# Optimization experiments

Hardware: AMD Instinct MI355X
Metric: run time of the kernel (lower is better)

Reference implementation:

```python
import jax, jax.numpy as jnp
import numpy as np

B, S, D = 8, 2048, 1024          # batch, seq, d_model
E, H = 32, 128                   # n_experts_ffn, d_expert_ffn
SHARED, K = 2, 4                 # n_expert_shared_ffn, k_ffn (routed top-k)
R = E - SHARED                   # n_expert_routed_ffn


def setup_inputs() -> dict:
    key = jax.random.key(0)
    ks = jax.random.split(key, 5)
    token_stream = jax.random.normal(ks[0], (B, S, D), jnp.float32)
    selection_input = jax.random.normal(ks[1], (B, S, D), jnp.float32)
    # init scaling mirrors reset_parameters (std_scale = 1)
    keys = jax.random.normal(ks[2], (E, D, H), jnp.float32) / np.sqrt(D)
    values = jax.random.normal(ks[3], (E, H, D), jnp.float32) / np.sqrt(E * H)
    expert_sel = jax.random.normal(ks[4], (E, D), jnp.float32) / np.sqrt(D)
    bias_ffn = jnp.zeros((E,), jnp.float32)
    return {
        "token_stream": token_stream,
        "selection_input": selection_input,
        "keys": keys,
        "values": values,
        "expert_sel": expert_sel,
        "bias_ffn": bias_ffn,
    }


def reference(token_stream, selection_input, keys, values, expert_sel, bias_ffn):
    # Router: sigmoid affinity over all experts. [B,S,E]
    affinity = jax.nn.sigmoid(jnp.einsum("bsd,ed->bse", selection_input, expert_sel))

    # Top-k over routed experts only (bias-corrected scores pick INDICES only).
    routed_scores = affinity[..., :R] + bias_ffn[:R]
    _, sel_routed = jax.lax.top_k(routed_scores, K)            # [B,S,K] int32
    shared = jnp.broadcast_to(jnp.arange(R, E, dtype=sel_routed.dtype),
                              sel_routed.shape[:-1] + (SHARED,))
    sel = jnp.concatenate([sel_routed, shared], axis=-1)        # [B,S,K+SHARED]

    # Gather the (unbiased) affinities of the selected experts.
    aff_sel = jnp.take_along_axis(affinity, sel, axis=-1)       # [B,S,K+SHARED]

    # Per-token dense combine weight over experts: w[b,s,e] = affinity if e selected else 0.
    # (selected indices are distinct: topk indices in [0,R), shared in [R,E))
    w = jnp.sum(jax.nn.one_hot(sel, E, dtype=affinity.dtype) * aff_sel[..., None],
                axis=-2)                                        # [B,S,E]

    # Expert FFN: cvmm(x, sel, keys) -> silu -> cvmm(., sel, values) weighted by affinity.
    # Dense-masked equivalent: compute all experts, zero out unselected via w.
    h = jax.nn.silu(jnp.einsum("bsd,edh->bseh", token_stream, keys))  # [B,S,E,H]
    out = jnp.einsum("bseh,bse,ehd->bsd", h, w, values)               # [B,S,D]
    return out, sel
```

## Files before the change

### kernel.cpp

```cpp
#include <hip/hip_runtime.h>
#include <math.h>

#define NTOK   16384
#define DDIM   1024
#define HDIM   128
#define NEXP   32
#define NROUTE 30
#define TOPK   4
#define TS     64
#define NJOBS_F 1696
#define CPX_F   212
#define SLAB   ((size_t)NTOK * DDIM)

typedef short bf16x8 __attribute__((ext_vector_type(8)));
typedef float f32x16 __attribute__((ext_vector_type(16)));
typedef unsigned int u32x4 __attribute__((ext_vector_type(4)));
typedef unsigned short u16;

__device__ __forceinline__ float sigmoidf_(float x) { return 1.f / (1.f + expf(-x)); }

__device__ __forceinline__ u16 f2bf(float x) {
  unsigned u = __float_as_uint(x);
  u += 0x7fffu + ((u >> 16) & 1u);
  return (u16)(u >> 16);
}
__device__ __forceinline__ float bf2f(u16 v) {
  return __uint_as_float(((unsigned)v) << 16);
}

__device__ __forceinline__ f32x16 mfma32(uint4 a, uint4 b, f32x16 c) {
  union { uint4 u; bf16x8 h; } A, B;
  A.u = a; B.u = b;
  return __builtin_amdgcn_mfma_f32_32x32x16_bf16(A.h, B.h, c, 0, 0, 0);
}

__device__ __forceinline__ void gload16(const void* g, void* l) {
  __builtin_amdgcn_global_load_lds(
      (const __attribute__((address_space(1))) unsigned int*)g,
      (__attribute__((address_space(3))) unsigned int*)l, 16, 0, 0);
}

__device__ __forceinline__ void lgkm_bar() {
  asm volatile("s_waitcnt lgkmcnt(0)\ns_barrier" ::: "memory");
}

__global__ __launch_bounds__(256) void prep_all_kernel(
    const float* __restrict__ X, u16* __restrict__ Xb,
    const float* __restrict__ K, u16* __restrict__ Kf,
    const float* __restrict__ V, u16* __restrict__ Vf)
{
  __shared__ float t[128][129];
  const int tid = threadIdx.x;
  int b = blockIdx.x;

  if (b < 4096) {
    const size_t base = ((size_t)b * 256 + tid) * 16;
    u16 v[16];
#pragma unroll
    for (int i = 0; i < 4; ++i) {
      const float4 f = *(const float4*)(X + base + i * 4);
      v[i*4+0] = f2bf(f.x); v[i*4+1] = f2bf(f.y);
      v[i*4+2] = f2bf(f.z); v[i*4+3] = f2bf(f.w);
    }
    *(uint4*)(Xb + base) = *(const uint4*)v;
    *(uint4*)(Xb + base + 8) = *(const uint4*)(v + 8);
    return;
  }
  b -= 4096;
  if (b < 256) {
    const int kc = b & 7, e = b >> 3;
#pragma unroll
    for (int i = 0; i < 64; ++i) {
      const int g = tid + i * 256;
      const int d = g >> 7, h = g & 127;
      t[d][h] = K[((size_t)e * DDIM + kc * 128 + d) * HDIM + h];
    }
    __syncthreads();
    u16* dst = Kf + ((size_t)e * 8 + kc) * 16384;
#pragma unroll
    for (int i = 0; i < 64; ++i) {
      const int f = tid + i * 256;
      const int s = f >> 11, wn = (f >> 9) & 3, l = (f >> 3) & 63, j = f & 7;
      const int khalf = l >> 5, l31 = l & 31;
      dst[f] = f2bf(t[(s * 2 + khalf) * 8 + j][wn * 32 + l31]);
    }
    return;
  }
  b -= 256;
  {
    const int dc = b & 7, e = b >> 3;
#pragma unroll
    for (int i = 0; i < 64; ++i) {
      const int g = tid + i * 256;
      const int h = g >> 7, dl = g & 127;
      t[h][dl] = V[((size_t)e * HDIM + h) * DDIM + dc * 128 + dl];
    }
    __syncthreads();
    u16* dst = Vf + ((size_t)e * 8 + dc) * 16384;
#pragma unroll
    for (int i = 0; i < 64; ++i) {
      const int f = tid + i * 256;
      const int s = f >> 11, wn = (f >> 9) & 3, l = (f >> 3) & 63, j = f & 7;
      const int khalf = l >> 5, l31 = l & 31;
      dst[f] = f2bf(t[(s * 2 + khalf) * 8 + j][wn * 32 + l31]);
    }
  }
}

__global__ __launch_bounds__(256, 4) void router_kernel(
    const float* __restrict__ SI, const float* __restrict__ ES,
    const float* __restrict__ bias, float* __restrict__ out_sel,
    float* __restrict__ w6, int* __restrict__ sel_e, int* __restrict__ counts)
{
  __shared__ float pbuf[4][32][65];
  __shared__ float aff[16][33];
  const int tid = threadIdx.x, wave = tid >> 6, lane = tid & 63;
  const int tok0 = blockIdx.x * 16 + wave * 4;

  float x[4][16];
#pragma unroll
  for (int t = 0; t < 4; ++t) {
    const float* xp = SI + (size_t)(tok0 + t) * DDIM + lane * 16;
#pragma unroll
    for (int q = 0; q < 4; ++q) {
      const float4 v = *(const float4*)(xp + q * 4);
      x[t][q*4+0]=v.x; x[t][q*4+1]=v.y; x[t][q*4+2]=v.z; x[t][q*4+3]=v.w;
    }
  }

#pragma unroll
  for (int g = 0; g < 4; ++g) {
#pragma unroll
    for (int ei = 0; ei < 8; ++ei) {
      const int e = g * 8 + ei;
      float es[16];
      const float* ep = ES + (size_t)e * DDIM + lane * 16;
#pragma unroll
      for (int q = 0; q < 4; ++q) {
        const float4 v = *(const float4*)(ep + q * 4);
        es[q*4+0]=v.x; es[q*4+1]=v.y; es[q*4+2]=v.z; es[q*4+3]=v.w;
      }
#pragma unroll
      for (int t = 0; t < 4; ++t) {
        float p = 0.f;
#pragma unroll
        for (int u = 0; u < 16; ++u) p = fmaf(x[t][u], es[u], p);
        pbuf[wave][ei * 4 + t][lane] = p;
      }
    }
    const int pr = lane & 31, hf = lane >> 5;
    const float* src = &pbuf[wave][pr][hf * 32];
    float4 s4 = make_float4(0.f, 0.f, 0.f, 0.f);
#pragma unroll
    for (int j = 0; j < 8; ++j) {
      const float4 v = *(const float4*)(src + j * 4);
      s4.x += v.x; s4.y += v.y; s4.z += v.z; s4.w += v.w;
    }
    float s = (s4.x + s4.y) + (s4.z + s4.w);
    s += __shfl_xor(s, 32, 64);
    if (hf == 0) aff[wave * 4 + (pr & 3)][g * 8 + (pr >> 2)] = s;
  }

  if (lane < 4) {
    const int tok = tok0 + lane;
    float af[NEXP];
#pragma unroll
    for (int e2 = 0; e2 < NEXP; ++e2)
      af[e2] = sigmoidf_(aff[wave * 4 + lane][e2]);
    float sc[NROUTE];
#pragma unroll
    for (int e2 = 0; e2 < NROUTE; ++e2) sc[e2] = af[e2] + bias[e2];
    unsigned used = 0u;
    int idx[6];
#pragma unroll
    for (int j = 0; j < TOPK; ++j) {
      float bv = -1e30f; int best = 0;
#pragma unroll
      for (int e2 = 0; e2 < NROUTE; ++e2)
        if (!((used >> e2) & 1u) && sc[e2] > bv) { bv = sc[e2]; best = e2; }
      used |= (1u << best);
      idx[j] = best;
    }
    idx[4] = 30; idx[5] = 31;
#pragma unroll
    for (int j = 0; j < 6; ++j) {
      out_sel[(size_t)tok * 6 + j] = (float)idx[j];
      w6[(size_t)tok * 6 + j] = af[idx[j]];
    }
#pragma unroll
    for (int j = 0; j < TOPK; ++j) {
      sel_e[(size_t)tok * TOPK + j] = idx[j];
      atomicAdd(&counts[j * NEXP + idx[j]], 1);
    }
  }
}

__global__ __launch_bounds__(256) void scan_kernel(const int* __restrict__ counts,
                                                   int* __restrict__ offsets,
                                                   int4* __restrict__ jm)
{
  __shared__ int c4[30][4];
  __shared__ int off4[30][4];
  __shared__ int nch[32];
  __shared__ int joff[31];
  const int tid = threadIdx.x;

  if (tid < 4) {
    int off = 0;
    for (int e = 0; e < NROUTE; ++e) {
      const int c = counts[tid * NEXP + e];
      offsets[tid * NEXP + e] = off;
      c4[e][tid] = c; off4[e][tid] = off;
      off += c;
    }
  }
  __syncthreads();
  if (tid < NROUTE) {
    int n = 0;
#pragma unroll
    for (int r = 0; r < 4; ++r) n += (c4[tid][r] + TS - 1) / TS;
    nch[tid] = n;
  }
  __syncthreads();
  if (tid == 0) {
    int run = 0;
    for (int e = 0; e < NROUTE; ++e) { joff[e] = run; run += nch[e]; }
    joff[NROUTE] = run;
  }
  __syncthreads();
  const int rt = joff[NROUTE];

  if (tid < NROUTE) {
    const int e = tid;
    int idx = joff[e];
    for (int r = 0; r < 4; ++r) {
      const int c = c4[e][r];
      for (int ch = 0; ch * TS < c; ++ch)
        jm[idx++] = make_int4(e, off4[e][r] + ch * TS, min(TS, c - ch * TS), r);
    }
  }
  for (int i = tid; i < 512; i += 256)
    jm[rt + i] = make_int4(30 + (i >> 8), (i & 255) * TS, TS, 4 + (i >> 8));
  for (int i = rt + 512 + tid; i < NJOBS_F; i += 256)
    jm[i] = make_int4(0, 0, 0, 0);
}

__global__ __launch_bounds__(256) void scatter_kernel(
    const int* __restrict__ sel_e, const float* __restrict__ w6,
    const int* __restrict__ offsets, int* __restrict__ cursor,
    int* __restrict__ list_tok, float* __restrict__ list_w)
{
  const int t = blockIdx.x * 256 + threadIdx.x;
  if (t >= NTOK) return;
#pragma unroll
  for (int j = 0; j < TOPK; ++j) {
    const int e   = sel_e[(size_t)t * TOPK + j];
    const int pos = atomicAdd(&cursor[j * NEXP + e], 1);
    const int dst = j * NTOK + offsets[j * NEXP + e] + pos;
    list_tok[dst] = t;
    list_w[dst]   = w6[(size_t)t * 6 + j];
  }
  list_tok[4 * NTOK + t] = t; list_w[4 * NTOK + t] = w6[(size_t)t * 6 + 4];
  list_tok[5 * NTOK + t] = t; list_w[5 * NTOK + t] = w6[(size_t)t * 6 + 5];
}

__device__ __forceinline__ void loadb(uint4* b, const u16* __restrict__ base,
                                      int c, int wid, int lane) {
#pragma unroll
  for (int s = 0; s < 8; ++s)
    b[s] = *(const uint4*)(base + (size_t)(((c * 8 + s) * 4 + wid) * 512) + lane * 8);
}

__global__ __launch_bounds__(256, 2) void ffn_kernel(
    const u16* __restrict__ Xb, const u16* __restrict__ Kf, const u16* __restrict__ Vf,
    const int4* __restrict__ jm, const int* __restrict__ list_tok,
    const float* __restrict__ list_w, u16* __restrict__ part)
{
  __shared__ __align__(16) u16 Xs[2][8192];
  __shared__ __align__(16) u16 Hs[TS * 128];
  __shared__ int   s_tok[TS];
  __shared__ float s_w[TS];

  const int bid = blockIdx.x;
  const int4 J = jm[(bid & 7) * CPX_F + (bid >> 3)];
  const int nrow = J.z;
  if (nrow == 0) return;
  const int e = J.x, base = J.y, rank = J.w;
  const int tid = threadIdx.x;
  const int wid = tid >> 6, lane = tid & 63;
  const int l31 = lane & 31, khalf = lane >> 5;
  const int sx = l31 & 15;

  const u16* Kf_e = Kf + (size_t)e * 131072;
  const u16* Vf_e = Vf + (size_t)e * 131072;
  const int*   lt  = list_tok + rank * NTOK + base;
  const float* lww = list_w  + rank * NTOK + base;

  size_t srcoff[4];
#pragma unroll
  for (int u = 0; u < 4; ++u) {
    const int r  = wid * 16 + u * 4 + (lane >> 4);
    const int rr = (r < nrow) ? r : 0;
    srcoff[u] = (size_t)lt[rr] * DDIM + (size_t)(((lane & 15) ^ (r & 15)) << 3);
  }

  #define STAGE_A(kc_, buf_) do { \
    _Pragma("unroll") \
    for (int u_ = 0; u_ < 4; ++u_) \
      gload16(Xb + srcoff[u_] + (kc_) * 128, &Xs[buf_][(wid * 16 + u_ * 4) * 128]); \
  } while (0)

  uint4 bb[2][8];
  STAGE_A(0, 0);
  loadb(bb[0], Kf_e, 0, wid, lane);

  if (tid < TS) {
    int t = 0; float w = 0.f;
    if (tid < nrow) { t = lt[tid]; w = lww[tid]; }
    s_tok[tid] = t; s_w[tid] = w;
  }
  lgkm_bar();

  f32x16 acc0, acc1;
#pragma unroll
  for (int i = 0; i < 16; ++i) { acc0[i] = 0.f; acc1[i] = 0.f; }

#pragma unroll
  for (int kc = 0; kc < 8; ++kc) {
    const int cur = kc & 1;
    asm volatile("s_barrier" ::: "memory");
    __builtin_amdgcn_sched_barrier(0);
    if (kc < 7) { STAGE_A(kc + 1, cur ^ 1); loadb(bb[cur ^ 1], Kf_e, kc + 1, wid, lane); }
    else        { loadb(bb[cur ^ 1], Vf_e, 0, wid, lane); }
    if (kc < 7) asm volatile("s_waitcnt vmcnt(12)" ::: "memory");
    else        asm volatile("s_waitcnt vmcnt(8)"  ::: "memory");
    asm volatile("s_barrier" ::: "memory");
    __builtin_amdgcn_sched_barrier(0);
#pragma unroll
    for (int s = 0; s < 8; ++s) {
      const int so = (((s * 2 + khalf) ^ sx) << 3);
      const uint4 a0 = *(const uint4*)(&Xs[cur][l31 * 128 + so]);
      const uint4 a1 = *(const uint4*)(&Xs[cur][(32 + l31) * 128 + so]);
      acc0 = mfma32(a0, bb[cur][s], acc0);
      acc1 = mfma32(a1, bb[cur][s], acc1);
    }
  }

  {
    const int hcol = wid * 32 + l31;
#pragma unroll
    for (int r = 0; r < 16; ++r) {
      const int row0 = (r & 3) + 8 * (r >> 2) + 4 * khalf;
      float v0 = acc0[r];
      v0 = v0 / (1.f + expf(-v0)) * s_w[row0];
      Hs[row0 * 128 + ((((hcol >> 3) ^ (row0 & 15)) << 3) | (hcol & 7))] = f2bf(v0);
      const int row1 = row0 + 32;
      float v1 = acc1[r];
      v1 = v1 / (1.f + expf(-v1)) * s_w[row1];
      Hs[row1 * 128 + ((((hcol >> 3) ^ (row1 & 15)) << 3) | (hcol & 7))] = f2bf(v1);
    }
  }
  lgkm_bar();

  uint4 a20[8], a21[8];
#pragma unroll
  for (int s = 0; s < 8; ++s) {
    a20[s] = *(const uint4*)(Hs + l31 * 128 + (((s * 2 + khalf) ^ sx) << 3));
    a21[s] = *(const uint4*)(Hs + (32 + l31) * 128 + (((s * 2 + khalf) ^ sx) << 3));
  }

  unsigned ob0[16], ob1[16]; bool ov0[16], ov1[16];
#pragma unroll
  for (int r = 0; r < 16; ++r) {
    const int row0 = (r & 3) + 8 * (r >> 2) + 4 * khalf;
    const int row1 = row0 + 32;
    ov0[r] = row0 < nrow; ov1[r] = row1 < nrow;
    ob0[r] = (unsigned)s_tok[row0] * DDIM;
    ob1[r] = (unsigned)s_tok[row1] * DDIM;
  }

  u16* pp = part + (size_t)rank * SLAB;

#pragma unroll
  for (int dc = 0; dc < 8; ++dc) {
    const int cur = dc & 1;
    if (dc < 7) loadb(bb[cur ^ 1], Vf_e, dc + 1, wid, lane);
    f32x16 o0, o1;
#pragma unroll
    for (int i = 0; i < 16; ++i) { o0[i] = 0.f; o1[i] = 0.f; }
#pragma unroll
    for (int s = 0; s < 8; ++s) {
      o0 = mfma32(a20[s], bb[cur][s], o0);
      o1 = mfma32(a21[s], bb[cur][s], o1);
    }
    const int col = dc * 128 + wid * 32 + l31;
#pragma unroll
    for (int r = 0; r < 16; ++r) {
      if (ov0[r]) __builtin_nontemporal_store(f2bf(o0[r]), &pp[(size_t)ob0[r] + col]);
      if (ov1[r]) __builtin_nontemporal_store(f2bf(o1[r]), &pp[(size_t)ob1[r] + col]);
    }
  }
  #undef STAGE_A
}

__global__ __launch_bounds__(256) void reduce_kernel(const u16* __restrict__ part,
                                                     float* __restrict__ out)
{
  const size_t i8 = ((size_t)blockIdx.x * 256 + threadIdx.x) * 8;
  float s[8];
#pragma unroll
  for (int j = 0; j < 8; ++j) s[j] = 0.f;
#pragma unroll
  for (int r = 0; r < 6; ++r) {
    const u32x4 v = __builtin_nontemporal_load((const u32x4*)(part + r * SLAB + i8));
#pragma unroll
    for (int q = 0; q < 4; ++q) {
      s[q*2+0] += __uint_as_float((v[q] & 0xffffu) << 16);
      s[q*2+1] += __uint_as_float(v[q] & 0xffff0000u);
    }
  }
  float4 o0 = make_float4(s[0], s[1], s[2], s[3]);
  float4 o1 = make_float4(s[4], s[5], s[6], s[7]);
  *(float4*)(out + i8) = o0;
  *(float4*)(out + i8 + 4) = o1;
}

extern "C" void kernel_launch(void* const* d_in, const int* in_sizes, int n_in,
                              void* d_out, int out_size, void* d_ws, size_t ws_size,
                              hipStream_t stream)
{
  const float* X    = (const float*)d_in[0];
  const float* SI   = (const float*)d_in[1];
  const float* keys = (const float*)d_in[2];
  const float* vals = (const float*)d_in[3];
  const float* ES   = (const float*)d_in[4];
  const float* bias = (const float*)d_in[5];
  float* out = (float*)d_out;
  float* out_sel = out + SLAB;

  char* ws = (char*)d_ws;
  int*   counts   = (int*)(ws + 0);
  int*   cursor   = (int*)(ws + 512);
  int*   offsets  = (int*)(ws + 1024);
  int4*  jm       = (int4*)(ws + 2048);
  int*   list_tok = (int*)(ws + 57344);
  float* list_w   = (float*)(ws + 450560);
  float* w6       = (float*)(ws + 919552);
  int*   sel_e    = (int*)(ws + 1312768);
  u16*   Xb       = (u16*)(ws + 1576960);
  u16*   Kf       = (u16*)(ws + 35131392);
  u16*   Vf       = (u16*)(ws + 43520000);
  u16*   part     = (u16*)(ws + 51908608);

  hipMemsetAsync(counts, 0, 1024, stream);

  prep_all_kernel<<<4096 + 256 + 256, 256, 0, stream>>>(X, Xb, keys, Kf, vals, Vf);
  router_kernel<<<NTOK / 16, 256, 0, stream>>>(SI, ES, bias, out_sel, w6, sel_e, counts);
  scan_kernel<<<1, 256, 0, stream>>>(counts, offsets, jm);
  scatter_kernel<<<NTOK / 256, 256, 0, stream>>>(sel_e, w6, offsets, cursor, list_tok, list_w);
  ffn_kernel<<<NJOBS_F, 256, 0, stream>>>(Xb, Kf, Vf, jm, list_tok, list_w, part);
  reduce_kernel<<<SLAB / (256 * 8), 256, 0, stream>>>(part, out);
}
```

Before: 415.5 us.

## Fuse weight/activation prep and router into one interleaved kernel launch

Merges the bf16 conversion/repack kernel and the router kernel into a single launch, interleaving one router block for every nine prep blocks so both memory-bound phases run concurrently. The router now processes 8 tokens per wave instead of 4, halving expert-selection weight reloads per token. Removes a kernel launch and the serialization tail between the two stages, at the cost of higher register use and a larger shared LDS buffer that may cut occupancy.

```diff
diff --git a/kernel.cpp b/kernel.cpp
--- a/kernel.cpp
+++ b/kernel.cpp
@@ -11,6 +11,7 @@
 #define NJOBS_F 1696
 #define CPX_F   212
 #define SLAB   ((size_t)NTOK * DDIM)
+#define NB_FUSED 5120
 
 typedef short bf16x8 __attribute__((ext_vector_type(8)));
 typedef float f32x16 __attribute__((ext_vector_type(16)));
@@ -44,14 +45,105 @@
   asm volatile("s_waitcnt lgkmcnt(0)\ns_barrier" ::: "memory");
 }
 
-__global__ __launch_bounds__(256) void prep_all_kernel(
+__global__ __launch_bounds__(256, 2) void prep_router_kernel(
     const float* __restrict__ X, u16* __restrict__ Xb,
     const float* __restrict__ K, u16* __restrict__ Kf,
-    const float* __restrict__ V, u16* __restrict__ Vf)
-{
-  __shared__ float t[128][129];
+    const float* __restrict__ V, u16* __restrict__ Vf,
+    const float* __restrict__ SI, const float* __restrict__ ES,
+    const float* __restrict__ bias, float* __restrict__ out_sel,
+    float* __restrict__ w6, int* __restrict__ sel_e, int* __restrict__ counts)
+{
+  __shared__ __align__(16) char lds[66048];
   const int tid = threadIdx.x;
-  int b = blockIdx.x;
+
+  if ((blockIdx.x % 10) == 9) {
+    const int rb = blockIdx.x / 10;
+    const int wave = tid >> 6, lane = tid & 63;
+    const int tok0 = rb * 32 + wave * 8;
+    float (*pbuf)[65] = ((float (*)[65])lds) + wave * 32;
+    float (*aff)[33]  = (float (*)[33])(lds + 33280);
+
+    float x[8][16];
+#pragma unroll
+    for (int t = 0; t < 8; ++t) {
+      const float* xp = SI + (size_t)(tok0 + t) * DDIM + lane * 16;
+#pragma unroll
+      for (int q = 0; q < 4; ++q) {
+        const float4 v = *(const float4*)(xp + q * 4);
+        x[t][q*4+0]=v.x; x[t][q*4+1]=v.y; x[t][q*4+2]=v.z; x[t][q*4+3]=v.w;
+      }
+    }
+
+#pragma unroll
+    for (int g = 0; g < 8; ++g) {
+#pragma unroll
+      for (int ei = 0; ei < 4; ++ei) {
+        const int e = g * 4 + ei;
+        float es[16];
+        const float* ep = ES + (size_t)e * DDIM + lane * 16;
+#pragma unroll
+        for (int q = 0; q < 4; ++q) {
+          const float4 v = *(const float4*)(ep + q * 4);
+          es[q*4+0]=v.x; es[q*4+1]=v.y; es[q*4+2]=v.z; es[q*4+3]=v.w;
+        }
+#pragma unroll
+        for (int t = 0; t < 8; ++t) {
+          float p = 0.f;
+#pragma unroll
+          for (int u = 0; u < 16; ++u) p = fmaf(x[t][u], es[u], p);
+          pbuf[ei * 8 + t][lane] = p;
+        }
+      }
+      const int pr = lane & 31, hf = lane >> 5;
+      const float* src = &pbuf[pr][hf * 32];
+      float4 s4 = make_float4(0.f, 0.f, 0.f, 0.f);
+#pragma unroll
+      for (int j = 0; j < 8; ++j) {
+        const float4 v = *(const float4*)(src + j * 4);
+        s4.x += v.x; s4.y += v.y; s4.z += v.z; s4.w += v.w;
+      }
+      float s = (s4.x + s4.y) + (s4.z + s4.w);
+      s += __shfl_xor(s, 32, 64);
+      if (hf == 0) aff[wave * 8 + (pr & 7)][g * 4 + (pr >> 3)] = s;
+    }
+
+    if (lane < 8) {
+      const int tok = tok0 + lane;
+      float af[NEXP];
+#pragma unroll
+      for (int e2 = 0; e2 < NEXP; ++e2)
+        af[e2] = sigmoidf_(aff[wave * 8 + lane][e2]);
+      float sc[NROUTE];
+#pragma unroll
+      for (int e2 = 0; e2 < NROUTE; ++e2) sc[e2] = af[e2] + bias[e2];
+      unsigned used = 0u;
+      int idx[6];
+#pragma unroll
+      for (int j = 0; j < TOPK; ++j) {
+        float bv = -1e30f; int best = 0;
+#pragma unroll
+        for (int e2 = 0; e2 < NROUTE; ++e2)
+          if (!((used >> e2) & 1u) && sc[e2] > bv) { bv = sc[e2]; best = e2; }
+        used |= (1u << best);
+        idx[j] = best;
+      }
+      idx[4] = 30; idx[5] = 31;
+#pragma unroll
+      for (int j = 0; j < 6; ++j) {
+        out_sel[(size_t)tok * 6 + j] = (float)idx[j];
+        w6[(size_t)tok * 6 + j] = af[idx[j]];
+      }
+#pragma unroll
+      for (int j = 0; j < TOPK; ++j) {
+        sel_e[(size_t)tok * TOPK + j] = idx[j];
+        atomicAdd(&counts[j * NEXP + idx[j]], 1);
+      }
+    }
+    return;
+  }
+
+  int b = blockIdx.x - (blockIdx.x + 1) / 10;
+  float (*t)[129] = (float (*)[129])lds;
 
   if (b < 4096) {
     const size_t base = ((size_t)b * 256 + tid) * 16;
@@ -103,94 +195,6 @@
       const int s = f >> 11, wn = (f >> 9) & 3, l = (f >> 3) & 63, j = f & 7;
       const int khalf = l >> 5, l31 = l & 31;
       dst[f] = f2bf(t[(s * 2 + khalf) * 8 + j][wn * 32 + l31]);
-    }
-  }
-}
-
-__global__ __launch_bounds__(256, 4) void router_kernel(
-    const float* __restrict__ SI, const float* __restrict__ ES,
-    const float* __restrict__ bias, float* __restrict__ out_sel,
-    float* __restrict__ w6, int* __restrict__ sel_e, int* __restrict__ counts)
-{
-  __shared__ float pbuf[4][32][65];
-  __shared__ float aff[16][33];
-  const int tid = threadIdx.x, wave = tid >> 6, lane = tid & 63;
-  const int tok0 = blockIdx.x * 16 + wave * 4;
-
-  float x[4][16];
-#pragma unroll
-  for (int t = 0; t < 4; ++t) {
-    const float* xp = SI + (size_t)(tok0 + t) * DDIM + lane * 16;
-#pragma unroll
-    for (int q = 0; q < 4; ++q) {
-      const float4 v = *(const float4*)(xp + q * 4);
-      x[t][q*4+0]=v.x; x[t][q*4+1]=v.y; x[t][q*4+2]=v.z; x[t][q*4+3]=v.w;
-    }
-  }
-
-#pragma unroll
-  for (int g = 0; g < 4; ++g) {
-#pragma unroll
-    for (int ei = 0; ei < 8; ++ei) {
-      const int e = g * 8 + ei;
-      float es[16];
-      const float* ep = ES + (size_t)e * DDIM + lane * 16;
-#pragma unroll
-      for (int q = 0; q < 4; ++q) {
-        const float4 v = *(const float4*)(ep + q * 4);
-        es[q*4+0]=v.x; es[q*4+1]=v.y; es[q*4+2]=v.z; es[q*4+3]=v.w;
-      }
-#pragma unroll
-      for (int t = 0; t < 4; ++t) {
-        float p = 0.f;
-#pragma unroll
-        for (int u = 0; u < 16; ++u) p = fmaf(x[t][u], es[u], p);
-        pbuf[wave][ei * 4 + t][lane] = p;
-      }
-    }
-    const int pr = lane & 31, hf = lane >> 5;
-    const float* src = &pbuf[wave][pr][hf * 32];
-    float4 s4 = make_float4(0.f, 0.f, 0.f, 0.f);
-#pragma unroll
-    for (int j = 0; j < 8; ++j) {
-      const float4 v = *(const float4*)(src + j * 4);
-      s4.x += v.x; s4.y += v.y; s4.z += v.z; s4.w += v.w;
-    }
-    float s = (s4.x + s4.y) + (s4.z + s4.w);
-    s += __shfl_xor(s, 32, 64);
-    if (hf == 0) aff[wave * 4 + (pr & 3)][g * 8 + (pr >> 2)] = s;
-  }
-
-  if (lane < 4) {
-    const int tok = tok0 + lane;
-    float af[NEXP];
-#pragma unroll
-    for (int e2 = 0; e2 < NEXP; ++e2)
-      af[e2] = sigmoidf_(aff[wave * 4 + lane][e2]);
-    float sc[NROUTE];
-#pragma unroll
-    for (int e2 = 0; e2 < NROUTE; ++e2) sc[e2] = af[e2] + bias[e2];
-    unsigned used = 0u;
-    int idx[6];
-#pragma unroll
-    for (int j = 0; j < TOPK; ++j) {
-      float bv = -1e30f; int best = 0;
-#pragma unroll
-      for (int e2 = 0; e2 < NROUTE; ++e2)
-        if (!((used >> e2) & 1u) && sc[e2] > bv) { bv = sc[e2]; best = e2; }
-      used |= (1u << best);
-      idx[j] = best;
-    }
-    idx[4] = 30; idx[5] = 31;
-#pragma unroll
-    for (int j = 0; j < 6; ++j) {
-      out_sel[(size_t)tok * 6 + j] = (float)idx[j];
-      w6[(size_t)tok * 6 + j] = af[idx[j]];
-    }
-#pragma unroll
-    for (int j = 0; j < TOPK; ++j) {
-      sel_e[(size_t)tok * TOPK + j] = idx[j];
-      atomicAdd(&counts[j * NEXP + idx[j]], 1);
     }
   }
 }
@@ -454,8 +458,9 @@
 
   hipMemsetAsync(counts, 0, 1024, stream);
 
-  prep_all_kernel<<<4096 + 256 + 256, 256, 0, stream>>>(X, Xb, keys, Kf, vals, Vf);
-  router_kernel<<<NTOK / 16, 256, 0, stream>>>(SI, ES, bias, out_sel, w6, sel_e, counts);
+  prep_router_kernel<<<NB_FUSED, 256, 0, stream>>>(X, Xb, keys, Kf, vals, Vf,
+                                                   SI, ES, bias, out_sel, w6,
+                                                   sel_e, counts);
   scan_kernel<<<1, 256, 0, stream>>>(counts, offsets, jm);
   scatter_kernel<<<NTOK / 256, 256, 0, stream>>>(sel_e, w6, offsets, cursor, list_tok, list_w);
   ffn_kernel<<<NJOBS_F, 256, 0, stream>>>(Xb, Kf, Vf, jm, list_tok, list_w, part);
```

New measurement: 398.8 us. -4.0%, faster.
